# Performance work log

Hardware: AMD Instinct MI355X
Metric: run time of the kernel (lower is better)

The kernel has to match this reference:

```python
import jax, jax.numpy as jnp
import numpy as np

# ---- static config (mirrors TALoss(num_classes=80, reg_max=16, strides=[8,16,32])) ----
B, M, NC, REG_MAX = 32, 20, 80, 16
STRIDES = (8, 16, 32)
HW = ((80, 80), (40, 40), (20, 20))          # feature map sizes for 640x640 input
NO = REG_MAX * 4 + NC                         # 144 channels per head
A = sum(h * w for h, w in HW)                 # 8400 anchors
TOPK, ALPHA, BETA = 10, 0.5, 6.0
BOX_G, CLS_G, DFL_G = 7.5, 0.5, 1.5
EPS = 1e-9


def setup_inputs() -> dict:
    key = jax.random.key(0)
    ks = jax.random.split(key, 6)
    feats = {f"feat{i}": jax.random.normal(ks[i], (B, NO, h, w), jnp.float32)
             for i, (h, w) in enumerate(HW)}
    # targets: (N,6) rows of (img_idx, class, cx, cy, w, h), normalized, 20 boxes/image, sorted by image
    img_idx = jnp.repeat(jnp.arange(B, dtype=jnp.float32), M)
    cls = jax.random.randint(ks[3], (B * M,), 0, NC).astype(jnp.float32)
    cxy = jax.random.uniform(ks[4], (B * M, 2), minval=0.2, maxval=0.8)
    wh = jax.random.uniform(ks[5], (B * M, 2), minval=0.05, maxval=0.3)
    targets = jnp.concatenate([img_idx[:, None], cls[:, None], cxy, wh], axis=1)
    return {**feats, "targets": targets}


def _make_anchors():
    pts, strs = [], []
    for (h, w), s in zip(HW, STRIDES):
        sx = jnp.arange(w, dtype=jnp.float32) + 0.5
        sy = jnp.arange(h, dtype=jnp.float32) + 0.5
        gy, gx = jnp.meshgrid(sy, sx, indexing="ij")
        pts.append(jnp.stack([gx, gy], -1).reshape(-1, 2))
        strs.append(jnp.full((h * w, 1), float(s), jnp.float32))
    return jnp.concatenate(pts), jnp.concatenate(strs)   # (A,2), (A,1)


def _ciou(b1, b2, eps=1e-7):
    # b1, b2: broadcastable xyxy boxes (..., 4) -> CIoU (...,)
    b1x1, b1y1, b1x2, b1y2 = b1[..., 0], b1[..., 1], b1[..., 2], b1[..., 3]
    b2x1, b2y1, b2x2, b2y2 = b2[..., 0], b2[..., 1], b2[..., 2], b2[..., 3]
    w1, h1 = b1x2 - b1x1, b1y2 - b1y1 + eps
    w2, h2 = b2x2 - b2x1, b2y2 - b2y1 + eps
    inter = (jnp.clip(jnp.minimum(b1x2, b2x2) - jnp.maximum(b1x1, b2x1), 0)
             * jnp.clip(jnp.minimum(b1y2, b2y2) - jnp.maximum(b1y1, b2y1), 0))
    union = w1 * h1 + w2 * h2 - inter + eps
    iou = inter / union
    cw = jnp.maximum(b1x2, b2x2) - jnp.minimum(b1x1, b2x1)
    ch = jnp.maximum(b1y2, b2y2) - jnp.minimum(b1y1, b2y1)
    c2 = cw ** 2 + ch ** 2 + eps
    rho2 = ((b2x1 + b2x2 - b1x1 - b1x2) ** 2 + (b2y1 + b2y2 - b1y1 - b1y2) ** 2) / 4.0
    v = (4.0 / np.pi ** 2) * (jnp.arctan(w2 / h2) - jnp.arctan(w1 / h1)) ** 2
    a = jax.lax.stop_gradient(v / (v - iou + (1.0 + eps)))   # torch: computed under no_grad
    return iou - (rho2 / c2 + v * a)


def _assign(pd_scores, pd_bboxes, anc, gt_labels, gt_bboxes, mask_gt):
    """TaskAlignedAssigner. pd_scores (B,A,NC) sigmoid-ed, pd_bboxes (B,A,4) image units,
    anc (A,2) image units, gt_labels (B,M), gt_bboxes (B,M,4), mask_gt (B,M) float."""
    # anchors inside each gt box -> (B,M,A)
    lt = anc[None, None, :, :] - gt_bboxes[:, :, None, :2]
    rb = gt_bboxes[:, :, None, 2:] - anc[None, None, :, :]
    mask_in = (jnp.concatenate([lt, rb], -1).min(-1) > EPS).astype(jnp.float32)
    mask = mask_in * mask_gt[..., None]                      # (B,M,A) candidate mask
    overlaps = jnp.clip(_ciou(gt_bboxes[:, :, None, :], pd_bboxes[:, None, :, :]), 0) * mask
    labels = gt_labels.astype(jnp.int32)                     # (B,M)
    # scores of each gt's class at every anchor: (B,M,A)
    bbox_scores = jnp.take_along_axis(pd_scores.transpose(0, 2, 1),
                                      jnp.broadcast_to(labels[:, :, None], (B, M, A)), axis=1) * mask
    align = (bbox_scores ** ALPHA) * (overlaps ** BETA)      # (B,M,A), already zero off-mask
    # top-k anchors per gt
    _, idxs = jax.lax.top_k(align, TOPK)                     # (B,M,K)
    idxs = jnp.where(mask_gt[..., None] > 0, idxs, 0)
    cnt = jax.nn.one_hot(idxs, A, dtype=jnp.float32).sum(-2)  # (B,M,A)
    mask_topk = jnp.where(cnt > 1, 0.0, cnt)
    mask_pos = mask_topk * mask
    # resolve anchors matched to multiple gts: keep the max-overlap gt
    fg = mask_pos.sum(1)                                     # (B,A)
    is_max = jnp.moveaxis(jax.nn.one_hot(overlaps.argmax(1), M, dtype=jnp.float32), -1, 1)  # (B,M,A)
    mask_pos = jnp.where(fg[:, None, :] > 1, is_max, mask_pos)
    fg = mask_pos.sum(1)
    tgt_idx = mask_pos.argmax(1)                             # (B,A)
    t_labels = jnp.take_along_axis(labels, tgt_idx, 1)       # (B,A)
    t_bboxes = jnp.take_along_axis(gt_bboxes, tgt_idx[..., None], 1)  # (B,A,4)
    fg_b = (fg > 0).astype(jnp.float32)
    t_scores = jax.nn.one_hot(t_labels, NC, dtype=jnp.float32) * fg_b[..., None]
    # normalize scores: align * (max overlap per gt) / (max align per gt)
    align_pos = align * mask_pos
    pos_align = align_pos.max(-1, keepdims=True)             # (B,M,1)
    pos_over = (overlaps * mask_pos).max(-1, keepdims=True)
    norm = (align_pos * pos_over / (pos_align + EPS)).max(1)  # (B,A)
    return t_bboxes, t_scores * norm[..., None], fg_b


def _forward(feat0, feat1, feat2, targets):
    feats = [feat0, feat1, feat2]
    pred = jnp.concatenate([f.reshape(B, NO, -1) for f in feats], axis=2)
    pred_distri = pred[:, :REG_MAX * 4].transpose(0, 2, 1)   # (B,A,64)
    pred_scores = pred[:, REG_MAX * 4:].transpose(0, 2, 1)   # (B,A,NC)
    anc, stride_t = _make_anchors()
    img_h, img_w = HW[0][0] * STRIDES[0], HW[0][1] * STRIDES[0]
    scale = jnp.array([img_w, img_h, img_w, img_h], jnp.float32)
    # ---- preprocess targets (N,6) -> padded (B,M,5), xywh*scale -> xyxy ----
    idx = targets[:, 0].astype(jnp.int32)
    pos = jnp.arange(targets.shape[0]) - jnp.searchsorted(idx, idx, side="left")
    out = jnp.zeros((B, M, 5), jnp.float32).at[idx, pos].set(targets[:, 1:])
    gt_labels = out[..., 0]
    xywh = out[..., 1:5] * scale
    gt_bboxes = jnp.concatenate([xywh[..., :2] - xywh[..., 2:] / 2,
                                 xywh[..., :2] + xywh[..., 2:] / 2], -1)
    mask_gt = (gt_bboxes.sum(-1) > 0).astype(jnp.float32)    # (B,M)
    # ---- DFL bbox decode (feature-map units) ----
    proj = jnp.arange(REG_MAX, dtype=jnp.float32)
    dist = jax.nn.softmax(pred_distri.reshape(B, A, 4, REG_MAX), -1) @ proj  # (B,A,4) ltrb
    pred_bboxes = jnp.concatenate([anc - dist[..., :2], anc + dist[..., 2:]], -1)
    # ---- task-aligned assignment (on detached preds, image units) ----
    pd_scores = jax.lax.stop_gradient(jax.nn.sigmoid(pred_scores))
    pd_bboxes = jax.lax.stop_gradient(pred_bboxes) * stride_t
    target_bboxes, target_scores, fg_mask = _assign(pd_scores, pd_bboxes, anc * stride_t,
                                                    gt_labels, gt_bboxes, mask_gt)
    target_bboxes = target_bboxes / stride_t
    tss = jnp.maximum(target_scores.sum(), 1.0)
    # ---- BCE-with-logits classification loss (pos_weight=1) ----
    x, t = pred_scores, target_scores
    bce = jnp.maximum(x, 0) - x * t + jnp.log1p(jnp.exp(-jnp.abs(x)))
    loss_cls = bce.sum() / tss
    # ---- CIoU box loss + DFL, weighted by per-anchor target score sum on fg ----
    weight = target_scores.sum(-1) * fg_mask                 # (B,A)
    iou = _ciou(pred_bboxes, target_bboxes)
    loss_box = ((1.0 - iou) * weight).sum() / tss
    tltrb = jnp.clip(jnp.concatenate([anc - target_bboxes[..., :2],
                                      target_bboxes[..., 2:] - anc], -1),
                     0, REG_MAX - 1 - 0.01)                  # (B,A,4)
    logp = jax.nn.log_softmax(pred_distri.reshape(B, A, 4, REG_MAX), -1)
    tl = tltrb.astype(jnp.int32)
    wl = (tl + 1).astype(jnp.float32) - tltrb
    nll_l = -jnp.take_along_axis(logp, tl[..., None], -1)[..., 0]
    nll_r = -jnp.take_along_axis(logp, (tl + 1)[..., None], -1)[..., 0]
    dfl = (nll_l * wl + nll_r * (1.0 - wl)).mean(-1)         # (B,A)
    loss_dfl = (dfl * weight).sum() / tss
    losses = jnp.stack([loss_box * BOX_G, loss_cls * CLS_G, loss_dfl * DFL_G])
    return losses.sum() * B, jax.lax.stop_gradient(losses)


def reference(feat0, feat1, feat2, targets):
    return _forward(feat0, feat1, feat2, targets)
```

## Files before the change

### kernel.cpp

```cpp
#include <hip/hip_runtime.h>
#include <math.h>

constexpr int BB  = 32;
constexpr int MM  = 20;
constexpr int NCC = 80;
constexpr int RM  = 16;
constexpr int NOC = 144;
constexpr int AT  = 8400;
constexpr int TK  = 10;
constexpr int BA  = BB * AT;
constexpr int BM  = BB * MM;
constexpr int MAXPOS = BM * TK;
constexpr int NSLOT = 1024;
constexpr int NTILE = 100 + 25 + 7;
constexpr float EPS_A = 1e-9f;
constexpr float VCOEF = 0.40528473456935108577551785283891f;

struct Lvl { const float* f; int o, w, hw; float s; };

__device__ inline Lvl level_of(int a, const float* f0, const float* f1, const float* f2){
  Lvl L;
  if (a < 6400)      { L.f = f0; L.o = a;        L.w = 80; L.hw = 6400; L.s = 8.f;  }
  else if (a < 8000) { L.f = f1; L.o = a - 6400; L.w = 40; L.hw = 1600; L.s = 16.f; }
  else               { L.f = f2; L.o = a - 8000; L.w = 20; L.hw = 400;  L.s = 32.f; }
  return L;
}

__device__ inline float frcp(float x){ return __builtin_amdgcn_rcpf(x); }

__device__ inline float fast_atan(float x){
  float ax = fabsf(x);
  bool big = ax > 1.f;
  float z = big ? frcp(ax) : ax;
  float z2 = z * z;
  float p = fmaf(z2, -0.0117212f, 0.0526533f);
  p = fmaf(z2, p, -0.1164329f);
  p = fmaf(z2, p, 0.1935435f);
  p = fmaf(z2, p, -0.3326235f);
  p = fmaf(z2, p, 0.9999773f);
  float r = z * p;
  r = big ? 1.57079632679f - r : r;
  return copysignf(r, x);
}

__device__ inline float ciou_f(float b1x1,float b1y1,float b1x2,float b1y2,
                               float b2x1,float b2y1,float b2x2,float b2y2){
  const float eps = 1e-7f;
  float w1 = b1x2 - b1x1, h1 = b1y2 - b1y1 + eps;
  float w2 = b2x2 - b2x1, h2 = b2y2 - b2y1 + eps;
  float iw = fmaxf(fminf(b1x2, b2x2) - fmaxf(b1x1, b2x1), 0.f);
  float ih = fmaxf(fminf(b1y2, b2y2) - fmaxf(b1y1, b2y1), 0.f);
  float inter = iw * ih;
  float uni = w1 * h1 + w2 * h2 - inter + eps;
  float iou = inter * frcp(uni);
  float cw = fmaxf(b1x2, b2x2) - fminf(b1x1, b2x1);
  float ch = fmaxf(b1y2, b2y2) - fminf(b1y1, b2y1);
  float c2 = cw * cw + ch * ch + eps;
  float dx = b2x1 + b2x2 - b1x1 - b1x2;
  float dy = b2y1 + b2y2 - b1y1 - b1y2;
  float rho2 = (dx * dx + dy * dy) * 0.25f;
  float r1 = w1 * frcp(h1), r2 = w2 * frcp(h2);
  float dat = fast_atan((r2 - r1) * frcp(fmaf(r1, r2, 1.f)));
  float v = VCOEF * dat * dat;
  float alpha = v * frcp(v - iou + (1.0f + eps));
  return iou - (rho2 * frcp(c2) + v * alpha);
}

__device__ inline unsigned long long shfl_xor_u64(unsigned long long v, int mask){
  int lo = __shfl_xor((int)(unsigned)(v & 0xFFFFFFFFull), mask);
  int hi = __shfl_xor((int)(unsigned)(v >> 32), mask);
  return ((unsigned long long)(unsigned)hi << 32) | (unsigned)lo;
}

__device__ inline float softplus4(float4 v){
  float s = fmaxf(v.x, 0.f) + __logf(1.f + __expf(-fabsf(v.x)));
  s += fmaxf(v.y, 0.f) + __logf(1.f + __expf(-fabsf(v.y)));
  s += fmaxf(v.z, 0.f) + __logf(1.f + __expf(-fabsf(v.z)));
  s += fmaxf(v.w, 0.f) + __logf(1.f + __expf(-fabsf(v.w)));
  return s;
}

__global__ void k_prep(const float* __restrict__ tgt, float* __restrict__ out5,
                       float* __restrict__ gtbox, int* __restrict__ gtlab,
                       float* __restrict__ gtmask, int* __restrict__ pa_i,
                       int* __restrict__ po_i, int* __restrict__ topk_arr,
                       double* __restrict__ acc){
  int t = threadIdx.x;
  for (int i = t; i < BM * 5; i += 640) out5[i] = 0.f;
  for (int i = t; i < MAXPOS; i += 640) topk_arr[i] = -1;
  if (t < 8) acc[t] = 0.0;
  pa_i[t] = 0; po_i[t] = 0;
  __syncthreads();
  {
    int img = (int)tgt[t * 6 + 0];
    int j = t;
    while (j > 0 && (int)tgt[(j - 1) * 6 + 0] == img) j--;
    int pos = t - j;
    if (img >= 0 && img < BB && pos < MM){
      for (int k = 0; k < 5; k++)
        out5[(img * MM + pos) * 5 + k] = tgt[t * 6 + 1 + k];
    }
  }
  __syncthreads();
  {
    float lab = out5[t * 5 + 0];
    float cx = out5[t * 5 + 1] * 640.f;
    float cy = out5[t * 5 + 2] * 640.f;
    float w  = out5[t * 5 + 3] * 640.f;
    float h  = out5[t * 5 + 4] * 640.f;
    float x1 = cx - w * 0.5f, y1 = cy - h * 0.5f;
    float x2 = cx + w * 0.5f, y2 = cy + h * 0.5f;
    gtbox[t * 4 + 0] = x1; gtbox[t * 4 + 1] = y1;
    gtbox[t * 4 + 2] = x2; gtbox[t * 4 + 3] = y2;
    gtlab[t] = (int)lab;
    gtmask[t] = ((x1 + y1 + x2 + y2) > 0.f) ? 1.f : 0.f;
  }
}

template<int HW, int W, int AOFF>
__device__ inline float feat_tile(const float* __restrict__ f, int b, int tile,
                                  float4* __restrict__ pbox, float4* __restrict__ lseg,
                                  unsigned* __restrict__ mpos,
                                  float (*sT)[65], float (*sD)[64], float (*sL)[64]){
  int tid = threadIdx.x;
  int o0 = tile * 64;
  int nA = HW - o0; if (nA > 64) nA = 64;
  const float* base = f + (size_t)b * NOC * HW + o0;
  float sp = 0.f;
  const float* cb = base + (size_t)(4 * RM) * HW;
#pragma unroll
  for (int k = 0; k < 5; k++){
    int idx = k * 256 + tid;
    int ch = idx >> 4, f4i = idx & 15;
    if (f4i * 4 < nA)
      sp += softplus4(*(const float4*)(cb + (size_t)ch * HW + f4i * 4));
  }
#pragma unroll
  for (int k = 0; k < 4; k++){
    int idx = k * 256 + tid;
    int ch = idx >> 4, f4i = idx & 15;
    if (f4i * 4 < nA){
      float4 v = *(const float4*)(base + (size_t)ch * HW + f4i * 4);
      sT[ch][f4i * 4 + 0] = v.x; sT[ch][f4i * 4 + 1] = v.y;
      sT[ch][f4i * 4 + 2] = v.z; sT[ch][f4i * 4 + 3] = v.w;
    }
  }
  __syncthreads();
  int anc = tid & 63, side = tid >> 6;
  if (anc < nA){
    float xs[16];
    xs[0] = sT[side * 16][anc];
    float mx = xs[0];
#pragma unroll
    for (int j = 1; j < 16; j++){ xs[j] = sT[side * 16 + j][anc]; mx = fmaxf(mx, xs[j]); }
    float sm = 0.f, dt = 0.f;
#pragma unroll
    for (int j = 0; j < 16; j++){
      float e = __expf(xs[j] - mx);
      sm += e; dt = fmaf(e, (float)j, dt);
    }
    sD[side][anc] = dt * frcp(sm);
    sL[side][anc] = mx + __logf(sm);
  }
  __syncthreads();
  if (tid < nA){
    int o = o0 + tid;
    int iy = o / W;
    float ax = (float)(o - iy * W) + 0.5f;
    float ay = (float)iy + 0.5f;
    int gi = b * AT + AOFF + o;
    pbox[gi] = make_float4(ax - sD[0][tid], ay - sD[1][tid],
                           ax + sD[2][tid], ay + sD[3][tid]);
    lseg[gi] = make_float4(sL[0][tid], sL[1][tid], sL[2][tid], sL[3][tid]);
  } else if (tid >= 64 && tid - 64 < nA){
    mpos[(size_t)b * AT + AOFF + o0 + (tid - 64)] = 0u;
  }
  return sp;
}

__global__ __launch_bounds__(256) void k_feat(
    const float* __restrict__ f0, const float* __restrict__ f1,
    const float* __restrict__ f2,
    float4* __restrict__ pbox, float4* __restrict__ lse,
    unsigned* __restrict__ mpos, double* __restrict__ acc){
  __shared__ float sT[64][65];
  __shared__ float sD[4][64];
  __shared__ float sL[4][64];
  int blk = blockIdx.x;
  int b = blk / NTILE, t = blk - b * NTILE;
  float sp;
  if (t < 100)      sp = feat_tile<6400, 80, 0>   (f0, b, t,        pbox, lse, mpos, sT, sD, sL);
  else if (t < 125) sp = feat_tile<1600, 40, 6400>(f1, b, t - 100,  pbox, lse, mpos, sT, sD, sL);
  else              sp = feat_tile< 400, 20, 8000>(f2, b, t - 125,  pbox, lse, mpos, sT, sD, sL);
  for (int off = 32; off; off >>= 1) sp += __shfl_down(sp, off);
  __shared__ float red[4];
  int wid = threadIdx.x >> 6, lid = threadIdx.x & 63;
  if (lid == 0) red[wid] = sp;
  __syncthreads();
  if (threadIdx.x == 0)
    atomicAdd(&acc[4], (double)(red[0] + red[1] + red[2] + red[3]));
}

__global__ __launch_bounds__(256) void k_align(
    const float* __restrict__ f0, const float* __restrict__ f1,
    const float* __restrict__ f2, const float4* __restrict__ pbox,
    const float* __restrict__ gtbox, const int* __restrict__ gtlab,
    const float* __restrict__ gtmask,
    unsigned* __restrict__ mpos, int* __restrict__ topk_arr){
  int pair = blockIdx.x;
  int b = pair / MM, m = pair % MM;
  if (gtmask[pair] <= 0.f) return;
  int tid = threadIdx.x;
  float gx1 = gtbox[pair * 4 + 0], gy1 = gtbox[pair * 4 + 1];
  float gx2 = gtbox[pair * 4 + 2], gy2 = gtbox[pair * 4 + 3];
  int lab = gtlab[pair];
  __shared__ float s_val[NSLOT];
  __shared__ int   s_anc[NSLOT];
  __shared__ unsigned long long s_red[4];
  __shared__ int   s_win[TK];
  int base = 0;

#define PROC_LEVEL(FPTR, W, HW, AOFF, S)                                      \
  {                                                                           \
    const float s_ = (S); const float inv_ = 1.f / (S);                       \
    int x0 = max(0, (int)floorf(gx1 * inv_ - 0.5f));                          \
    int x1 = min((W) - 1, (int)ceilf(gx2 * inv_ - 0.5f));                     \
    int y0 = max(0, (int)floorf(gy1 * inv_ - 0.5f));                          \
    int y1 = min((W) - 1, (int)ceilf(gy2 * inv_ - 0.5f));                     \
    int nxx = x1 - x0 + 1, nyy = y1 - y0 + 1;                                 \
    if (nxx > 0 && nyy > 0){                                                  \
      int ntot = nxx * nyy;                                                   \
      unsigned magic = 0xFFFFFFFFu / (unsigned)nxx + 1u;                      \
      const float* clsrow = (FPTR) + (size_t)b * NOC * (HW)                   \
                            + (size_t)(4 * RM + lab) * (HW);                  \
      for (int t = tid; t < ntot; t += 256){                                  \
        int slot = base + t;                                                  \
        if (slot >= NSLOT) break;                                             \
        int iy = (int)(((unsigned long long)(unsigned)t * magic) >> 32);      \
        int ix = t - iy * nxx + x0;                                           \
        iy += y0;                                                             \
        float ax = ((float)ix + 0.5f) * s_;                                   \
        float ay = ((float)iy + 0.5f) * s_;                                   \
        float mn = fminf(fminf(ax - gx1, ay - gy1),                           \
                         fminf(gx2 - ax, gy2 - ay));                          \
        int o = iy * (W) + ix;                                                \
        int a = (AOFF) + o;                                                   \
        float aln = -1.f;                                                     \
        if (mn > EPS_A){                                                      \
          float4 pb = pbox[b * AT + a];                                       \
          float c = ciou_f(gx1, gy1, gx2, gy2,                                \
                           pb.x * s_, pb.y * s_, pb.z * s_, pb.w * s_);       \
          float ovl = fmaxf(c, 0.f);                                          \
          if (ovl > 0.f){                                                     \
            float xv = clsrow[o];                                             \
            float sc = frcp(1.f + __expf(-xv));                               \
            float o2 = ovl * ovl;                                             \
            aln = sqrtf(sc) * (o2 * o2 * o2);                                 \
          }                                                                   \
        }                                                                     \
        s_val[slot] = aln;                                                    \
        s_anc[slot] = a;                                                      \
      }                                                                       \
      base += ntot;                                                           \
    }                                                                         \
  }

  PROC_LEVEL(f0, 80, 6400, 0, 8.f)
  PROC_LEVEL(f1, 40, 1600, 6400, 16.f)
  PROC_LEVEL(f2, 20, 400, 8000, 32.f)
#undef PROC_LEVEL

  __syncthreads();
  int total = min(base, NSLOT);
  int wid = tid >> 6, lid = tid & 63;
  for (int r = 0; r < TK; r++){
    unsigned long long key = 0ULL;
    for (int i = tid; i < total; i += 256){
      float v = s_val[i];
      if (v > 0.f){
        unsigned long long k2 =
            ((unsigned long long)__float_as_uint(v) << 32) |
            (unsigned long long)(0xFFFFFFFFu - (unsigned)i);
        key = key > k2 ? key : k2;
      }
    }
    for (int xm = 1; xm < 64; xm <<= 1){
      unsigned long long o = shfl_xor_u64(key, xm);
      key = key > o ? key : o;
    }
    if (lid == 0) s_red[wid] = key;
    __syncthreads();
    if (tid == 0){
      unsigned long long k = s_red[0];
      k = k > s_red[1] ? k : s_red[1];
      k = k > s_red[2] ? k : s_red[2];
      k = k > s_red[3] ? k : s_red[3];
      if (k){
        int slot = (int)(0xFFFFFFFFu - (unsigned)(k & 0xFFFFFFFFull));
        s_win[r] = s_anc[slot];
        s_val[slot] = -1.f;
      } else s_win[r] = -1;
    }
    __syncthreads();
  }
  if (tid < TK){
    int a = s_win[tid];
    topk_arr[pair * TK + tid] = a;
    if (a >= 0) atomicOr(&mpos[(size_t)b * AT + a], 1u << m);
  }
}

__global__ __launch_bounds__(256) void k_resolve(
    const float* __restrict__ f0, const float* __restrict__ f1,
    const float* __restrict__ f2, const float4* __restrict__ pbox,
    const float* __restrict__ gtbox, const int* __restrict__ gtlab,
    const float* __restrict__ gtmask, const unsigned* __restrict__ mpos,
    const int* __restrict__ topk_arr,
    unsigned char* __restrict__ resm, float* __restrict__ resaln,
    int* __restrict__ pa_i, int* __restrict__ po_i){
  int i = blockIdx.x * 256 + threadIdx.x;
  int a = topk_arr[i];
  if (a < 0) return;
  int pair = i / TK;
  int b = pair / MM, m = pair % MM;
  unsigned bits = mpos[(size_t)b * AT + a];
  if (m != __ffs(bits) - 1) return;
  Lvl L = level_of(a, f0, f1, f2);
  float ax = ((float)(L.o % L.w) + 0.5f) * L.s;
  float ay = ((float)(L.o / L.w) + 0.5f) * L.s;
  float4 pb = pbox[b * AT + a];
  float px1 = pb.x * L.s, py1 = pb.y * L.s, px2 = pb.z * L.s, py2 = pb.w * L.s;
  int mr; float ovl;
  if (__popc(bits) > 1){
    float best = -1.f; int bm = 0;
    for (int mm = 0; mm < MM; mm++){
      float v = 0.f;
      if (gtmask[b * MM + mm] > 0.f){
        float x1 = gtbox[(b * MM + mm) * 4 + 0], y1 = gtbox[(b * MM + mm) * 4 + 1];
        float x2 = gtbox[(b * MM + mm) * 4 + 2], y2 = gtbox[(b * MM + mm) * 4 + 3];
        float mn = fminf(fminf(ax - x1, ay - y1), fminf(x2 - ax, y2 - ay));
        if (mn > EPS_A)
          v = fmaxf(ciou_f(x1, y1, x2, y2, px1, py1, px2, py2), 0.f);
      }
      if (v > best){ best = v; bm = mm; }
    }
    mr = bm; ovl = fmaxf(best, 0.f);
  } else {
    mr = m;
    float x1 = gtbox[(b * MM + mr) * 4 + 0], y1 = gtbox[(b * MM + mr) * 4 + 1];
    float x2 = gtbox[(b * MM + mr) * 4 + 2], y2 = gtbox[(b * MM + mr) * 4 + 3];
    ovl = fmaxf(ciou_f(x1, y1, x2, y2, px1, py1, px2, py2), 0.f);
  }
  int lab = gtlab[b * MM + mr];
  float xv = L.f[(size_t)b * NOC * L.hw + (size_t)(4 * RM + lab) * L.hw + L.o];
  float sc = frcp(1.f + __expf(-xv));
  float o2 = ovl * ovl;
  float aln = sqrtf(sc) * (o2 * o2 * o2);
  size_t gi = (size_t)b * AT + a;
  resm[gi] = (unsigned char)mr;
  resaln[gi] = aln;
  atomicMax(&pa_i[b * MM + mr], __float_as_int(aln));
  atomicMax(&po_i[b * MM + mr], __float_as_int(ovl));
}

__global__ __launch_bounds__(256) void k_final(
    const float* __restrict__ f0, const float* __restrict__ f1,
    const float* __restrict__ f2,
    const float4* __restrict__ pbox, const float4* __restrict__ lse,
    const float* __restrict__ gtbox, const int* __restrict__ gtlab,
    const int* __restrict__ pa_i, const int* __restrict__ po_i,
    const unsigned* __restrict__ mpos, const int* __restrict__ topk_arr,
    const unsigned char* __restrict__ resm, const float* __restrict__ resaln,
    double* __restrict__ acc){
  int i = blockIdx.x * 256 + threadIdx.x;
  float w_ = 0.f, clsp = 0.f, boxp = 0.f, dflp = 0.f;
  int a = topk_arr[i];
  if (a >= 0){
    int pair = i / TK;
    int b = pair / MM, m = pair % MM;
    unsigned bits = mpos[(size_t)b * AT + a];
    if (m == __ffs(bits) - 1){
      size_t gi = (size_t)b * AT + a;
      int mr = (int)resm[gi];
      float aln = resaln[gi];
      float pa = __int_as_float(pa_i[b * MM + mr]);
      float po = __int_as_float(po_i[b * MM + mr]);
      w_ = aln * po * frcp(pa + EPS_A);
      Lvl L = level_of(a, f0, f1, f2);
      const float* base = L.f + (size_t)b * NOC * L.hw + L.o;
      float ax = (float)(L.o % L.w) + 0.5f;
      float ay = (float)(L.o / L.w) + 0.5f;
      float inv_s = frcp(L.s);
      float tx1 = gtbox[(b * MM + mr) * 4 + 0] * inv_s, ty1 = gtbox[(b * MM + mr) * 4 + 1] * inv_s;
      float tx2 = gtbox[(b * MM + mr) * 4 + 2] * inv_s, ty2 = gtbox[(b * MM + mr) * 4 + 3] * inv_s;
      float4 pb = pbox[b * AT + a];
      float iou = ciou_f(pb.x, pb.y, pb.z, pb.w, tx1, ty1, tx2, ty2);
      boxp = (1.f - iou) * w_;
      float4 L4 = lse[b * AT + a];
      float lsv[4] = { L4.x, L4.y, L4.z, L4.w };
      float tv[4] = { ax - tx1, ay - ty1, tx2 - ax, ty2 - ay };
      float dfl = 0.f;
#pragma unroll
      for (int s4 = 0; s4 < 4; s4++){
        float t = fminf(fmaxf(tv[s4], 0.f), (float)(RM - 1) - 0.01f);
        int tl = (int)t;
        float wl = (float)(tl + 1) - t;
        float xl = base[(size_t)(s4 * RM + tl) * L.hw];
        float xr = base[(size_t)(s4 * RM + tl + 1) * L.hw];
        dfl += (lsv[s4] - xl) * wl + (lsv[s4] - xr) * (1.f - wl);
      }
      dflp = dfl * 0.25f * w_;
      int lab = gtlab[b * MM + mr];
      clsp = base[(size_t)(4 * RM + lab) * L.hw] * w_;
    }
  }
  __shared__ float red[4][4];
  float vals[4] = { w_, clsp, boxp, dflp };
  int wid = threadIdx.x >> 6, lid = threadIdx.x & 63;
#pragma unroll
  for (int j = 0; j < 4; j++){
    float v = vals[j];
    for (int off = 32; off; off >>= 1) v += __shfl_down(v, off);
    if (lid == 0) red[wid][j] = v;
  }
  __syncthreads();
  if (threadIdx.x == 0){
    float t0 = 0.f, t1 = 0.f, t2 = 0.f, t3 = 0.f;
    for (int w2 = 0; w2 < 4; w2++){
      t0 += red[w2][0]; t1 += red[w2][1]; t2 += red[w2][2]; t3 += red[w2][3];
    }
    atomicAdd(&acc[0], (double)t0);
    atomicAdd(&acc[1], (double)t1);
    atomicAdd(&acc[2], (double)t2);
    atomicAdd(&acc[3], (double)t3);
  }
}

__global__ void k_out(const double* __restrict__ acc, float* __restrict__ out){
  if (threadIdx.x == 0 && blockIdx.x == 0){
    double tss = acc[0] > 1.0 ? acc[0] : 1.0;
    double loss_box = acc[2] / tss;
    double loss_cls = (acc[4] - acc[1]) / tss;
    double loss_dfl = acc[3] / tss;
    float l0 = (float)(loss_box * 7.5);
    float l1 = (float)(loss_cls * 0.5);
    float l2 = (float)(loss_dfl * 1.5);
    out[0] = (l0 + l1 + l2) * 32.f;
    out[1] = l0;
    out[2] = l1;
    out[3] = l2;
  }
}

extern "C" void kernel_launch(void* const* d_in, const int* in_sizes, int n_in,
                              void* d_out, int out_size, void* d_ws, size_t ws_size,
                              hipStream_t stream) {
  const float* f0 = (const float*)d_in[0];
  const float* f1 = (const float*)d_in[1];
  const float* f2 = (const float*)d_in[2];
  const float* tg = (const float*)d_in[3];
  float* out = (float*)d_out;

  char* w = (char*)d_ws;
  size_t off = 0;
  auto alloc = [&](size_t bytes) -> void* {
    void* p = w + off;
    off += (bytes + 255) & ~(size_t)255;
    return p;
  };
  float4*        pbox    = (float4*)       alloc((size_t)BA * 16);
  float4*        lse     = (float4*)       alloc((size_t)BA * 16);
  float*         gtbox   = (float*)        alloc((size_t)BM * 16);
  int*           gtlab   = (int*)          alloc((size_t)BM * 4);
  float*         gtmask  = (float*)        alloc((size_t)BM * 4);
  float*         out5    = (float*)        alloc((size_t)BM * 20);
  unsigned*      mpos    = (unsigned*)     alloc((size_t)BA * 4);
  int*           topk_arr= (int*)          alloc((size_t)MAXPOS * 4);
  unsigned char* resm    = (unsigned char*)alloc((size_t)BA);
  float*         resaln  = (float*)        alloc((size_t)BA * 4);
  int*           pa      = (int*)          alloc((size_t)BM * 4);
  int*           po      = (int*)          alloc((size_t)BM * 4);
  double*        acc     = (double*)       alloc(8 * 8);

  k_prep<<<1, 640, 0, stream>>>(tg, out5, gtbox, gtlab, gtmask, pa, po, topk_arr, acc);
  k_feat<<<BB * NTILE, 256, 0, stream>>>(f0, f1, f2, pbox, lse, mpos, acc);
  k_align<<<BM, 256, 0, stream>>>(f0, f1, f2, pbox, gtbox, gtlab, gtmask, mpos, topk_arr);
  k_resolve<<<MAXPOS / 256, 256, 0, stream>>>(f0, f1, f2, pbox, gtbox, gtlab, gtmask,
                                              mpos, topk_arr, resm, resaln, pa, po);
  k_final<<<MAXPOS / 256, 256, 0, stream>>>(f0, f1, f2, pbox, lse, gtbox, gtlab,
                                            pa, po, mpos, topk_arr, resm, resaln, acc);
  k_out<<<1, 64, 0, stream>>>(acc, out);
}
```

Measured before the change: 255.5 us.

## Split feature kernel into per-anchor decode and grid-stride BCE blocks, fuse prep

Replaces the tiled shared-memory feature kernel with a single launch whose blocks do one of three jobs: one-thread-per-anchor DFL decode, grid-stride softplus summation over the class channels into per-block partials, or target preparation (formerly a separate kernel). The BCE partials are reduced in the output kernel instead of through a double atomic. This removes one launch and the shared-memory transposes and syncs, and balances the memory streaming. In exchange, each decode thread makes 64 strided scalar loads.

```diff
diff --git a/kernel.cpp b/kernel.cpp
--- a/kernel.cpp
+++ b/kernel.cpp
@@ -12,9 +12,19 @@
 constexpr int BM  = BB * MM;
 constexpr int MAXPOS = BM * TK;
 constexpr int NSLOT = 1024;
-constexpr int NTILE = 100 + 25 + 7;
 constexpr float EPS_A = 1e-9f;
 constexpr float VCOEF = 0.40528473456935108577551785283891f;
+
+constexpr int NBOX0 = BB * 6400 / 256;
+constexpr int NBOX1 = BB * 1600 / 256;
+constexpr int NBOX2 = BB * 400 / 256;
+constexpr int NBOX  = NBOX0 + NBOX1 + NBOX2;
+constexpr int NBCE  = 2048;
+constexpr unsigned C0F4 = 80 * 6400 / 4;
+constexpr unsigned C1F4 = 80 * 1600 / 4;
+constexpr unsigned C2F4 = 80 * 400 / 4;
+constexpr unsigned CBF4 = C0F4 + C1F4 + C2F4;
+constexpr unsigned NF4  = (unsigned)BB * CBF4;
 
 struct Lvl { const float* f; int o, w, hw; float s; };
 
@@ -80,125 +90,113 @@
   return s;
 }
 
-__global__ void k_prep(const float* __restrict__ tgt, float* __restrict__ out5,
-                       float* __restrict__ gtbox, int* __restrict__ gtlab,
-                       float* __restrict__ gtmask, int* __restrict__ pa_i,
-                       int* __restrict__ po_i, int* __restrict__ topk_arr,
-                       double* __restrict__ acc){
-  int t = threadIdx.x;
-  for (int i = t; i < BM * 5; i += 640) out5[i] = 0.f;
-  for (int i = t; i < MAXPOS; i += 640) topk_arr[i] = -1;
-  if (t < 8) acc[t] = 0.0;
-  pa_i[t] = 0; po_i[t] = 0;
-  __syncthreads();
-  {
-    int img = (int)tgt[t * 6 + 0];
-    int j = t;
-    while (j > 0 && (int)tgt[(j - 1) * 6 + 0] == img) j--;
-    int pos = t - j;
-    if (img >= 0 && img < BB && pos < MM){
-      for (int k = 0; k < 5; k++)
-        out5[(img * MM + pos) * 5 + k] = tgt[t * 6 + 1 + k];
-    }
-  }
-  __syncthreads();
-  {
-    float lab = out5[t * 5 + 0];
-    float cx = out5[t * 5 + 1] * 640.f;
-    float cy = out5[t * 5 + 2] * 640.f;
-    float w  = out5[t * 5 + 3] * 640.f;
-    float h  = out5[t * 5 + 4] * 640.f;
-    float x1 = cx - w * 0.5f, y1 = cy - h * 0.5f;
-    float x2 = cx + w * 0.5f, y2 = cy + h * 0.5f;
-    gtbox[t * 4 + 0] = x1; gtbox[t * 4 + 1] = y1;
-    gtbox[t * 4 + 2] = x2; gtbox[t * 4 + 3] = y2;
-    gtlab[t] = (int)lab;
-    gtmask[t] = ((x1 + y1 + x2 + y2) > 0.f) ? 1.f : 0.f;
-  }
-}
-
 template<int HW, int W, int AOFF>
-__device__ inline float feat_tile(const float* __restrict__ f, int b, int tile,
-                                  float4* __restrict__ pbox, float4* __restrict__ lseg,
-                                  unsigned* __restrict__ mpos,
-                                  float (*sT)[65], float (*sD)[64], float (*sL)[64]){
-  int tid = threadIdx.x;
-  int o0 = tile * 64;
-  int nA = HW - o0; if (nA > 64) nA = 64;
-  const float* base = f + (size_t)b * NOC * HW + o0;
-  float sp = 0.f;
-  const float* cb = base + (size_t)(4 * RM) * HW;
+__device__ inline void decode_anchor(const float* __restrict__ f, int u,
+                                     float4* __restrict__ pbox,
+                                     float4* __restrict__ lseg,
+                                     unsigned* __restrict__ mpos){
+  int b = u / HW, o = u - b * HW;
+  const float* base = f + (size_t)b * NOC * HW + o;
+  float d[4], ls[4];
 #pragma unroll
-  for (int k = 0; k < 5; k++){
-    int idx = k * 256 + tid;
-    int ch = idx >> 4, f4i = idx & 15;
-    if (f4i * 4 < nA)
-      sp += softplus4(*(const float4*)(cb + (size_t)ch * HW + f4i * 4));
-  }
+  for (int side = 0; side < 4; side++){
+    float x[16];
 #pragma unroll
-  for (int k = 0; k < 4; k++){
-    int idx = k * 256 + tid;
-    int ch = idx >> 4, f4i = idx & 15;
-    if (f4i * 4 < nA){
-      float4 v = *(const float4*)(base + (size_t)ch * HW + f4i * 4);
-      sT[ch][f4i * 4 + 0] = v.x; sT[ch][f4i * 4 + 1] = v.y;
-      sT[ch][f4i * 4 + 2] = v.z; sT[ch][f4i * 4 + 3] = v.w;
-    }
-  }
-  __syncthreads();
-  int anc = tid & 63, side = tid >> 6;
-  if (anc < nA){
-    float xs[16];
-    xs[0] = sT[side * 16][anc];
-    float mx = xs[0];
+    for (int j = 0; j < 16; j++)
+      x[j] = base[(size_t)((side * 16 + j) * HW)];
+    float mx = x[0];
 #pragma unroll
-    for (int j = 1; j < 16; j++){ xs[j] = sT[side * 16 + j][anc]; mx = fmaxf(mx, xs[j]); }
+    for (int j = 1; j < 16; j++) mx = fmaxf(mx, x[j]);
     float sm = 0.f, dt = 0.f;
 #pragma unroll
     for (int j = 0; j < 16; j++){
-      float e = __expf(xs[j] - mx);
+      float e = __expf(x[j] - mx);
       sm += e; dt = fmaf(e, (float)j, dt);
     }
-    sD[side][anc] = dt * frcp(sm);
-    sL[side][anc] = mx + __logf(sm);
-  }
-  __syncthreads();
-  if (tid < nA){
-    int o = o0 + tid;
-    int iy = o / W;
-    float ax = (float)(o - iy * W) + 0.5f;
-    float ay = (float)iy + 0.5f;
-    int gi = b * AT + AOFF + o;
-    pbox[gi] = make_float4(ax - sD[0][tid], ay - sD[1][tid],
-                           ax + sD[2][tid], ay + sD[3][tid]);
-    lseg[gi] = make_float4(sL[0][tid], sL[1][tid], sL[2][tid], sL[3][tid]);
-  } else if (tid >= 64 && tid - 64 < nA){
-    mpos[(size_t)b * AT + AOFF + o0 + (tid - 64)] = 0u;
-  }
-  return sp;
-}
-
-__global__ __launch_bounds__(256) void k_feat(
+    d[side]  = dt * frcp(sm);
+    ls[side] = mx + __logf(sm);
+  }
+  int iy = o / W;
+  float ax = (float)(o - iy * W) + 0.5f;
+  float ay = (float)iy + 0.5f;
+  int gi = b * AT + AOFF + o;
+  pbox[gi] = make_float4(ax - d[0], ay - d[1], ax + d[2], ay + d[3]);
+  lseg[gi] = make_float4(ls[0], ls[1], ls[2], ls[3]);
+  mpos[gi] = 0u;
+}
+
+__global__ __launch_bounds__(256) void k_feat2(
     const float* __restrict__ f0, const float* __restrict__ f1,
-    const float* __restrict__ f2,
+    const float* __restrict__ f2, const float* __restrict__ tgt,
     float4* __restrict__ pbox, float4* __restrict__ lse,
-    unsigned* __restrict__ mpos, double* __restrict__ acc){
-  __shared__ float sT[64][65];
-  __shared__ float sD[4][64];
-  __shared__ float sL[4][64];
+    unsigned* __restrict__ mpos, double* __restrict__ bce_part,
+    float* __restrict__ out5, float* __restrict__ gtbox,
+    int* __restrict__ gtlab, float* __restrict__ gtmask,
+    int* __restrict__ pa_i, int* __restrict__ po_i,
+    int* __restrict__ topk_arr, double* __restrict__ acc){
+  __shared__ float red[4];
   int blk = blockIdx.x;
-  int b = blk / NTILE, t = blk - b * NTILE;
-  float sp;
-  if (t < 100)      sp = feat_tile<6400, 80, 0>   (f0, b, t,        pbox, lse, mpos, sT, sD, sL);
-  else if (t < 125) sp = feat_tile<1600, 40, 6400>(f1, b, t - 100,  pbox, lse, mpos, sT, sD, sL);
-  else              sp = feat_tile< 400, 20, 8000>(f2, b, t - 125,  pbox, lse, mpos, sT, sD, sL);
-  for (int off = 32; off; off >>= 1) sp += __shfl_down(sp, off);
-  __shared__ float red[4];
-  int wid = threadIdx.x >> 6, lid = threadIdx.x & 63;
-  if (lid == 0) red[wid] = sp;
-  __syncthreads();
-  if (threadIdx.x == 0)
-    atomicAdd(&acc[4], (double)(red[0] + red[1] + red[2] + red[3]));
+  int tid = threadIdx.x;
+  if (blk < NBOX){
+    if (blk < NBOX0){
+      decode_anchor<6400, 80, 0>(f0, blk * 256 + tid, pbox, lse, mpos);
+    } else if (blk < NBOX0 + NBOX1){
+      decode_anchor<1600, 40, 6400>(f1, (blk - NBOX0) * 256 + tid, pbox, lse, mpos);
+    } else {
+      decode_anchor<400, 20, 8000>(f2, (blk - NBOX0 - NBOX1) * 256 + tid, pbox, lse, mpos);
+    }
+  } else if (blk < NBOX + NBCE){
+    int bi = blk - NBOX;
+    float sp = 0.f;
+    for (unsigned i = (unsigned)bi * 256u + (unsigned)tid; i < NF4;
+         i += (unsigned)NBCE * 256u){
+      unsigned b = i / CBF4;
+      unsigned r = i - b * CBF4;
+      const float4* p;
+      if (r < C0F4)
+        p = (const float4*)(f0) + (size_t)b * (NOC * 6400 / 4) + (64 * 6400 / 4) + r;
+      else if (r < C0F4 + C1F4)
+        p = (const float4*)(f1) + (size_t)b * (NOC * 1600 / 4) + (64 * 1600 / 4) + (r - C0F4);
+      else
+        p = (const float4*)(f2) + (size_t)b * (NOC * 400 / 4) + (64 * 400 / 4) + (r - C0F4 - C1F4);
+      sp += softplus4(*p);
+    }
+    for (int off = 32; off; off >>= 1) sp += __shfl_down(sp, off);
+    int wid = tid >> 6, lid = tid & 63;
+    if (lid == 0) red[wid] = sp;
+    __syncthreads();
+    if (tid == 0) bce_part[bi] = (double)(red[0] + red[1] + red[2] + red[3]);
+  } else {
+    for (int i = tid; i < BM * 5; i += 256) out5[i] = 0.f;
+    for (int i = tid; i < MAXPOS; i += 256) topk_arr[i] = -1;
+    for (int i = tid; i < BM; i += 256){ pa_i[i] = 0; po_i[i] = 0; }
+    if (tid < 8) acc[tid] = 0.0;
+    __syncthreads();
+    for (int t = tid; t < BM; t += 256){
+      int img = (int)tgt[t * 6 + 0];
+      int j = t;
+      while (j > 0 && (int)tgt[(j - 1) * 6 + 0] == img) j--;
+      int pos = t - j;
+      if (img >= 0 && img < BB && pos < MM){
+        for (int k = 0; k < 5; k++)
+          out5[(img * MM + pos) * 5 + k] = tgt[t * 6 + 1 + k];
+      }
+    }
+    __syncthreads();
+    for (int t = tid; t < BM; t += 256){
+      float lab = out5[t * 5 + 0];
+      float cx = out5[t * 5 + 1] * 640.f;
+      float cy = out5[t * 5 + 2] * 640.f;
+      float w  = out5[t * 5 + 3] * 640.f;
+      float h  = out5[t * 5 + 4] * 640.f;
+      float x1 = cx - w * 0.5f, y1 = cy - h * 0.5f;
+      float x2 = cx + w * 0.5f, y2 = cy + h * 0.5f;
+      gtbox[t * 4 + 0] = x1; gtbox[t * 4 + 1] = y1;
+      gtbox[t * 4 + 2] = x2; gtbox[t * 4 + 3] = y2;
+      gtlab[t] = (int)lab;
+      gtmask[t] = ((x1 + y1 + x2 + y2) > 0.f) ? 1.f : 0.f;
+    }
+  }
 }
 
 __global__ __launch_bounds__(256) void k_align(
@@ -436,11 +434,23 @@
   }
 }
 
-__global__ void k_out(const double* __restrict__ acc, float* __restrict__ out){
-  if (threadIdx.x == 0 && blockIdx.x == 0){
+__global__ void k_out(const double* __restrict__ acc,
+                      const double* __restrict__ bce_part,
+                      float* __restrict__ out){
+  __shared__ double sd[256];
+  double s = 0.0;
+  for (int i = threadIdx.x; i < NBCE; i += 256) s += bce_part[i];
+  sd[threadIdx.x] = s;
+  __syncthreads();
+  for (int off = 128; off; off >>= 1){
+    if (threadIdx.x < off) sd[threadIdx.x] += sd[threadIdx.x + off];
+    __syncthreads();
+  }
+  if (threadIdx.x == 0){
+    double bce_sum = sd[0];
     double tss = acc[0] > 1.0 ? acc[0] : 1.0;
     double loss_box = acc[2] / tss;
-    double loss_cls = (acc[4] - acc[1]) / tss;
+    double loss_cls = (bce_sum - acc[1]) / tss;
     double loss_dfl = acc[3] / tss;
     float l0 = (float)(loss_box * 7.5);
     float l1 = (float)(loss_cls * 0.5);
@@ -481,13 +491,15 @@
   int*           pa      = (int*)          alloc((size_t)BM * 4);
   int*           po      = (int*)          alloc((size_t)BM * 4);
   double*        acc     = (double*)       alloc(8 * 8);
-
-  k_prep<<<1, 640, 0, stream>>>(tg, out5, gtbox, gtlab, gtmask, pa, po, topk_arr, acc);
-  k_feat<<<BB * NTILE, 256, 0, stream>>>(f0, f1, f2, pbox, lse, mpos, acc);
+  double*        bcep    = (double*)       alloc((size_t)NBCE * 8);
+
+  k_feat2<<<NBOX + NBCE + 1, 256, 0, stream>>>(f0, f1, f2, tg, pbox, lse, mpos, bcep,
+                                               out5, gtbox, gtlab, gtmask, pa, po,
+                                               topk_arr, acc);
   k_align<<<BM, 256, 0, stream>>>(f0, f1, f2, pbox, gtbox, gtlab, gtmask, mpos, topk_arr);
   k_resolve<<<MAXPOS / 256, 256, 0, stream>>>(f0, f1, f2, pbox, gtbox, gtlab, gtmask,
                                               mpos, topk_arr, resm, resaln, pa, po);
   k_final<<<MAXPOS / 256, 256, 0, stream>>>(f0, f1, f2, pbox, lse, gtbox, gtlab,
                                             pa, po, mpos, topk_arr, resm, resaln, acc);
-  k_out<<<1, 64, 0, stream>>>(acc, out);
-}
+  k_out<<<1, 256, 0, stream>>>(acc, bcep, out);
+}
```

Result: faster. 247.7 us (-3.0%).
